# Optimization experiments

Hardware: AMD Instinct MI355X
Metric: run time of the kernel (lower is better)

The kernel has to match this reference:

```python
import jax, jax.numpy as jnp
import numpy as np

N_NODES = 25000
N_EDGES = 400000
EMBED_DIM = 128
NUM_HEADS = 8
D_K = EMBED_DIM // NUM_HEADS


def setup_inputs() -> dict:
    key = jax.random.key(0)
    ks = jax.random.split(key, 8)
    sc = 1.0 / np.sqrt(EMBED_DIM)
    return {
        "x": jax.random.normal(ks[0], (N_NODES, EMBED_DIM), jnp.float32),
        "edge_index": jax.random.randint(ks[1], (2, N_EDGES), 0, N_NODES),
        "attn_bias": jax.random.normal(ks[2], (N_EDGES, NUM_HEADS), jnp.float32),
        "Wq": jax.random.normal(ks[3], (EMBED_DIM, EMBED_DIM), jnp.float32) * sc,
        "bq": jnp.zeros((EMBED_DIM,), jnp.float32),
        "Wk": jax.random.normal(ks[4], (EMBED_DIM, EMBED_DIM), jnp.float32) * sc,
        "bk": jnp.zeros((EMBED_DIM,), jnp.float32),
        "Wv": jax.random.normal(ks[5], (EMBED_DIM, EMBED_DIM), jnp.float32) * sc,
        "bv": jnp.zeros((EMBED_DIM,), jnp.float32),
        "Wo": jax.random.normal(ks[6], (EMBED_DIM, EMBED_DIM), jnp.float32) * sc,
        "bo": jnp.zeros((EMBED_DIM,), jnp.float32),
    }


def reference(x, edge_index, attn_bias, Wq, bq, Wk, bk, Wv, bv, Wo, bo):
    N = x.shape[0]
    E = edge_index.shape[1]
    H, dk = NUM_HEADS, D_K
    scale = 1.0 / np.sqrt(dk).astype(np.float32)
    dst = edge_index[0]  # query/aggregation node per edge
    src = edge_index[1]  # key/value node per edge

    # project at node level (as torch: linear(x)[index]), then gather per edge
    q = (x @ Wq.T + bq)[dst].reshape(E, H, dk)
    k = (x @ Wk.T + bk)[src].reshape(E, H, dk)
    v = (x @ Wv.T + bv)[src].reshape(E, H, dk)

    logits = scale * jnp.sum(q * k, axis=2) + attn_bias  # [E, H]

    # segment softmax over edges grouped by destination node
    m = jax.ops.segment_max(logits, dst, num_segments=N)     # [N, H]
    e = jnp.exp(logits - m[dst])                              # [E, H]
    z = jax.ops.segment_sum(e, dst, num_segments=N)           # [N, H]
    scores = e / z[dst]                                       # [E, H]

    agg = jax.ops.segment_sum(scores[..., None] * v, dst, num_segments=N)  # [N, H, dk]
    out = agg.reshape(N, H * dk) @ Wo.T + bo                   # [N, embed_dim]
    return out, logits[..., None]
```

## Files before the change

kernel.cpp:

```cpp
#include <hip/hip_runtime.h>
#include <math.h>

#define N_NODES 25000
#define N_EDGES 400000
#define EMBED   128
#define HEADS   8
#define DK      16
#define NBLK    98

typedef __attribute__((ext_vector_type(8))) short bf16x8;
typedef __attribute__((ext_vector_type(4))) float f32x4;
typedef unsigned int uint;
typedef unsigned short ushort;

__device__ inline uint pack2_bf16(float a, float b) {
    union { float f; uint u; } ua, ub;
    ua.f = a; ub.f = b;
    uint ra = (ua.u + 0x7FFFu + ((ua.u >> 16) & 1u)) >> 16;
    uint rb = (ub.u + 0x7FFFu + ((ub.u >> 16) & 1u)) >> 16;
    return (ra & 0xFFFFu) | (rb << 16);
}
__device__ inline ushort cvt_bf16(float a) {
    union { float f; uint u; } ua; ua.f = a;
    return (ushort)((ua.u + 0x7FFFu + ((ua.u >> 16) & 1u)) >> 16);
}
__device__ inline float bf16_lo(uint u) {
    union { uint u; float f; } x; x.u = u << 16; return x.f;
}
__device__ inline float bf16_hi(uint u) {
    union { uint u; float f; } x; x.u = u & 0xFFFF0000u; return x.f;
}

#define NX (N_NODES * 128)
__global__ __launch_bounds__(256) void convert_all(
    const float* __restrict__ x,
    const float* __restrict__ Wq, const float* __restrict__ Wk,
    const float* __restrict__ Wv, const float* __restrict__ Wo,
    ushort* __restrict__ xb, ushort* __restrict__ wb, int* __restrict__ deg)
{
    int i = blockIdx.x * 256 + threadIdx.x;
    if (i < N_NODES) deg[i] = 0;
    int base = i * 2;
    if (base < NX) {
        float2 v = *reinterpret_cast<const float2*>(x + base);
        reinterpret_cast<uint*>(xb)[i] = pack2_bf16(v.x, v.y);
    } else {
        int j = base - NX;
        if (j < 4 * 16384) {
            const float* src = (j < 16384) ? Wq + j
                             : (j < 32768) ? Wk + (j - 16384)
                             : (j < 49152) ? Wv + (j - 32768)
                             :               Wo + (j - 49152);
            float2 v = *reinterpret_cast<const float2*>(src);
            reinterpret_cast<uint*>(wb)[j >> 1] = pack2_bf16(v.x, v.y);
        }
    }
}

__global__ __launch_bounds__(256) void gemm_qkv_deg(
    const ushort* __restrict__ A, const ushort* __restrict__ Wall,
    const float* __restrict__ bq, const float* __restrict__ bk,
    const float* __restrict__ bv,
    ushort* __restrict__ Qb, ushort* __restrict__ KVu,
    const int* __restrict__ ei, int* __restrict__ deg,
    int M)
{
    const int which = blockIdx.y;
    if (which == 3) {
        int t = blockIdx.x * 256 + threadIdx.x;
        int e = t * 4;
        if (e + 3 < N_EDGES) {
            int4 d = *reinterpret_cast<const int4*>(ei + e);
            atomicAdd(&deg[d.x], 1);
            atomicAdd(&deg[d.y], 1);
            atomicAdd(&deg[d.z], 1);
            atomicAdd(&deg[d.w], 1);
        } else {
            for (; e < N_EDGES && e < t * 4 + 4; ++e)
                atomicAdd(&deg[ei[e]], 1);
        }
        return;
    }

    const ushort* W = Wall + which * 16384;
    const float* bias = (which == 0) ? bq : (which == 1) ? bk : bv;

    const int lane = threadIdx.x & 63;
    const int wave = threadIdx.x >> 6;
    const int ml   = lane & 15;
    const int quad = lane >> 4;
    const int m0   = blockIdx.x * 64 + wave * 16;

    int arow = m0 + ml; if (arow >= M) arow = M - 1;
    const ushort* ap = A + arow * 128 + quad * 8;

    f32x4 acc[8];
#pragma unroll
    for (int ct = 0; ct < 8; ++ct) acc[ct] = (f32x4){0.f, 0.f, 0.f, 0.f};

#pragma unroll
    for (int ks = 0; ks < 128; ks += 32) {
        bf16x8 af = *reinterpret_cast<const bf16x8*>(ap + ks);
#pragma unroll
        for (int ct = 0; ct < 8; ++ct) {
            bf16x8 bf = *reinterpret_cast<const bf16x8*>(
                W + (ct * 16 + ml) * 128 + ks + quad * 8);
            acc[ct] = __builtin_amdgcn_mfma_f32_16x16x32_bf16(af, bf, acc[ct], 0, 0, 0);
        }
    }

#pragma unroll
    for (int ct = 0; ct < 8; ++ct) {
        int col = ct * 16 + ml;
        float bv_ = bias[col];
#pragma unroll
        for (int r = 0; r < 4; ++r) {
            int row = m0 + quad * 4 + r;
            if (row >= M) continue;
            ushort v = cvt_bf16(acc[ct][r] + bv_);
            if (which == 0) {
                Qb[row * 128 + col] = v;
            } else {
                KVu[row * 256 + (col >> 1) * 4 + (col & 1) + ((which == 2) ? 2 : 0)] = v;
            }
        }
    }
}

__global__ __launch_bounds__(256) void gemm_out(
    const ushort* __restrict__ A, const ushort* __restrict__ W,
    const float* __restrict__ bias, float* __restrict__ C, int M)
{
    const int lane = threadIdx.x & 63;
    const int wave = threadIdx.x >> 6;
    const int ml   = lane & 15;
    const int quad = lane >> 4;
    const int m0   = blockIdx.x * 64 + wave * 16;

    int arow = m0 + ml; if (arow >= M) arow = M - 1;
    const ushort* ap = A + arow * 128 + quad * 8;

    f32x4 acc[8];
#pragma unroll
    for (int ct = 0; ct < 8; ++ct) acc[ct] = (f32x4){0.f, 0.f, 0.f, 0.f};

#pragma unroll
    for (int ks = 0; ks < 128; ks += 32) {
        bf16x8 af = *reinterpret_cast<const bf16x8*>(ap + ks);
#pragma unroll
        for (int ct = 0; ct < 8; ++ct) {
            bf16x8 bf = *reinterpret_cast<const bf16x8*>(
                W + (ct * 16 + ml) * 128 + ks + quad * 8);
            acc[ct] = __builtin_amdgcn_mfma_f32_16x16x32_bf16(af, bf, acc[ct], 0, 0, 0);
        }
    }

#pragma unroll
    for (int ct = 0; ct < 8; ++ct) {
        int col = ct * 16 + ml;
        float bv_ = bias[col];
#pragma unroll
        for (int r = 0; r < 4; ++r) {
            int row = m0 + quad * 4 + r;
            if (row < M)
                C[row * 128 + col] = acc[ct][r] + bv_;
        }
    }
}

__global__ __launch_bounds__(256) void scan_blocks(
    const int* __restrict__ deg, int* __restrict__ excl, int* __restrict__ bsum)
{
    __shared__ int sh[256];
    int t = threadIdx.x;
    int gid = blockIdx.x * 256 + t;
    int v = (gid < N_NODES) ? deg[gid] : 0;
    sh[t] = v;
    __syncthreads();
#pragma unroll
    for (int off = 1; off < 256; off <<= 1) {
        int u = (t >= off) ? sh[t - off] : 0;
        __syncthreads();
        sh[t] += u;
        __syncthreads();
    }
    if (gid < N_NODES) excl[gid] = sh[t] - v;
    if (t == 255) bsum[blockIdx.x] = sh[255];
}

__global__ __launch_bounds__(128) void scan_tops(
    const int* __restrict__ bsum, int* __restrict__ bbase)
{
    __shared__ int sh[128];
    int t = threadIdx.x;
    int v = (t < NBLK) ? bsum[t] : 0;
    sh[t] = v;
    __syncthreads();
#pragma unroll
    for (int off = 1; off < 128; off <<= 1) {
        int u = (t >= off) ? sh[t - off] : 0;
        __syncthreads();
        sh[t] += u;
        __syncthreads();
    }
    if (t < NBLK) bbase[t] = sh[t] - v;
}

__global__ __launch_bounds__(256) void scan_apply(
    int* __restrict__ excl, const int* __restrict__ bbase,
    int* __restrict__ cursor)
{
    int t = threadIdx.x;
    int gid = blockIdx.x * 256 + t;
    if (gid < N_NODES) {
        int o = excl[gid] + bbase[blockIdx.x];
        excl[gid] = o;
        cursor[gid] = o;
    }
    if (blockIdx.x == 0 && t == 0) excl[N_NODES] = N_EDGES;
}

__global__ __launch_bounds__(256) void scatter_edges(
    const int* __restrict__ ei, int* __restrict__ cursor,
    int2* __restrict__ csr2)
{
    int e = blockIdx.x * 256 + threadIdx.x;
    if (e >= N_EDGES) return;
    int dst = ei[e];
    int src = ei[N_EDGES + e];
    int pos = atomicAdd(&cursor[dst], 1);
    csr2[pos] = make_int2(e, src);
}

__global__ __launch_bounds__(256) void fused_attn(
    const ushort* __restrict__ Q2, const uint2* __restrict__ KV,
    const float* __restrict__ attn_bias,
    const int* __restrict__ offsets, const int2* __restrict__ csr2,
    float* __restrict__ logits, ushort* __restrict__ AGG)
{
    const int lane = threadIdx.x & 63;
    const int wid  = threadIdx.x >> 6;
    const int n = blockIdx.x * 4 + wid;
    const int start = offsets[n], end = offsets[n + 1];
    const int h = lane >> 3;

    uint qu = reinterpret_cast<const uint*>(Q2)[n * 64 + lane];
    float qx = bf16_lo(qu), qy = bf16_hi(qu);

    float z = 0.f, accx = 0.f, accy = 0.f;

    for (int base = start; base < end; base += 64) {
        int cnt = end - base; if (cnt > 64) cnt = 64;
        int e_l = 0, s_l = 0;
        if (lane < cnt) {
            int2 es = csr2[base + lane];
            e_l = es.x; s_l = es.y;
        }
        int j = 0;
        for (; j + 3 < cnt; j += 4) {
            int e0 = __shfl(e_l, j, 64),     e1 = __shfl(e_l, j + 1, 64);
            int e2 = __shfl(e_l, j + 2, 64), e3 = __shfl(e_l, j + 3, 64);
            int s0 = __shfl(s_l, j, 64),     s1 = __shfl(s_l, j + 1, 64);
            int s2 = __shfl(s_l, j + 2, 64), s3 = __shfl(s_l, j + 3, 64);
            uint2 kv0 = KV[s0 * 64 + lane], kv1 = KV[s1 * 64 + lane];
            uint2 kv2 = KV[s2 * 64 + lane], kv3 = KV[s3 * 64 + lane];
            float b0 = attn_bias[e0 * 8 + h], b1 = attn_bias[e1 * 8 + h];
            float b2 = attn_bias[e2 * 8 + h], b3 = attn_bias[e3 * 8 + h];

            float d0 = qx * bf16_lo(kv0.x) + qy * bf16_hi(kv0.x);
            float d1 = qx * bf16_lo(kv1.x) + qy * bf16_hi(kv1.x);
            float d2 = qx * bf16_lo(kv2.x) + qy * bf16_hi(kv2.x);
            float d3 = qx * bf16_lo(kv3.x) + qy * bf16_hi(kv3.x);
#pragma unroll
            for (int off = 1; off < 8; off <<= 1) {
                d0 += __shfl_xor(d0, off, 64);
                d1 += __shfl_xor(d1, off, 64);
                d2 += __shfl_xor(d2, off, 64);
                d3 += __shfl_xor(d3, off, 64);
            }
            float l0 = 0.25f * d0 + b0, l1 = 0.25f * d1 + b1;
            float l2 = 0.25f * d2 + b2, l3 = 0.25f * d3 + b3;
            if ((lane & 7) == 0) {
                logits[e0 * 8 + h] = l0;
                logits[e1 * 8 + h] = l1;
                logits[e2 * 8 + h] = l2;
                logits[e3 * 8 + h] = l3;
            }
            float p0 = __expf(l0), p1 = __expf(l1);
            float p2 = __expf(l2), p3 = __expf(l3);
            z += (p0 + p1) + (p2 + p3);
            accx += p0 * bf16_lo(kv0.y) + p1 * bf16_lo(kv1.y)
                  + p2 * bf16_lo(kv2.y) + p3 * bf16_lo(kv3.y);
            accy += p0 * bf16_hi(kv0.y) + p1 * bf16_hi(kv1.y)
                  + p2 * bf16_hi(kv2.y) + p3 * bf16_hi(kv3.y);
        }
        for (; j < cnt; ++j) {
            int e0 = __shfl(e_l, j, 64);
            int s0 = __shfl(s_l, j, 64);
            uint2 kv0 = KV[s0 * 64 + lane];
            float b0 = attn_bias[e0 * 8 + h];
            float d0 = qx * bf16_lo(kv0.x) + qy * bf16_hi(kv0.x);
#pragma unroll
            for (int off = 1; off < 8; off <<= 1) d0 += __shfl_xor(d0, off, 64);
            float l0 = 0.25f * d0 + b0;
            if ((lane & 7) == 0) logits[e0 * 8 + h] = l0;
            float p0 = __expf(l0);
            z += p0;
            accx += p0 * bf16_lo(kv0.y);
            accy += p0 * bf16_hi(kv0.y);
        }
    }

    float inv = (z > 0.f) ? 1.f / z : 0.f;
    reinterpret_cast<uint*>(AGG)[n * 64 + lane] = pack2_bf16(accx * inv, accy * inv);
}

extern "C" void kernel_launch(void* const* d_in, const int* in_sizes, int n_in,
                              void* d_out, int out_size, void* d_ws, size_t ws_size,
                              hipStream_t stream)
{
    const float* x         = (const float*)d_in[0];
    const int*   ei        = (const int*)  d_in[1];
    const float* attn_bias = (const float*)d_in[2];
    const float* Wq = (const float*)d_in[3];
    const float* bq = (const float*)d_in[4];
    const float* Wk = (const float*)d_in[5];
    const float* bk = (const float*)d_in[6];
    const float* Wv = (const float*)d_in[7];
    const float* bv = (const float*)d_in[8];
    const float* Wo = (const float*)d_in[9];
    const float* bo = (const float*)d_in[10];

    float* out    = (float*)d_out;
    float* logits = out + N_NODES * EMBED;

    ushort* xb   = (ushort*)d_ws;
    ushort* wb   = xb + NX;
    ushort* Qb   = wb + 4 * 16384;
    ushort* KVu  = Qb + NX;
    ushort* AGGb = KVu + 2 * NX;
    int* deg     = (int*)(AGGb + NX);
    int* offsets = deg + N_NODES;
    int* cursor  = offsets + N_NODES + 1;
    int2* csr2   = (int2*)(cursor + N_NODES);
    int* bsum    = (int*)(csr2 + N_EDGES);
    int* bbase   = bsum + NBLK;

    int npairs = (NX + 4 * 16384) / 2;
    convert_all<<<(npairs + 255) / 256, 256, 0, stream>>>(x, Wq, Wk, Wv, Wo, xb, wb, deg);

    int gblocks = (N_NODES + 63) / 64;
    dim3 qkvgrid(gblocks, 4);
    gemm_qkv_deg<<<qkvgrid, 256, 0, stream>>>(xb, wb, bq, bk, bv, Qb, KVu,
                                              ei, deg, N_NODES);

    scan_blocks<<<NBLK, 256, 0, stream>>>(deg, offsets, bsum);
    scan_tops<<<1, 128, 0, stream>>>(bsum, bbase);
    scan_apply<<<NBLK, 256, 0, stream>>>(offsets, bbase, cursor);
    scatter_edges<<<(N_EDGES + 255) / 256, 256, 0, stream>>>(ei, cursor, csr2);

    fused_attn<<<N_NODES / 4, 256, 0, stream>>>(Qb, (const uint2*)KVu, attn_bias,
                                                offsets, csr2, logits, AGGb);

    gemm_out<<<gblocks, 256, 0, stream>>>(AGGb, wb + 3 * 16384, bo, out, N_NODES);
}
```

Measured before the change: 214.0 us.

## Process eight edges per wave with per-head lanes and separate K/V buffers

Splits the interleaved KV buffer into separate K and V arrays and remaps fused_attn so each lane owns one head of one of eight concurrent edges. Each lane now loads a full 16-element K and V slice with 128-bit loads and computes the dot product locally, with no shuffle reduction per edge. Partial sums are combined once at the end with a transpose-style butterfly reduction. This removes per-edge shuffles and serial edge iteration, at the cost of more registers per lane and wasted lanes for nodes whose degree is not a multiple of eight.

```diff
diff --git a/kernel.cpp b/kernel.cpp
--- a/kernel.cpp
+++ b/kernel.cpp
@@ -61,7 +61,7 @@
     const ushort* __restrict__ A, const ushort* __restrict__ Wall,
     const float* __restrict__ bq, const float* __restrict__ bk,
     const float* __restrict__ bv,
-    ushort* __restrict__ Qb, ushort* __restrict__ KVu,
+    ushort* __restrict__ Qb, ushort* __restrict__ Kb, ushort* __restrict__ Vb,
     const int* __restrict__ ei, int* __restrict__ deg,
     int M)
 {
@@ -84,6 +84,7 @@
 
     const ushort* W = Wall + which * 16384;
     const float* bias = (which == 0) ? bq : (which == 1) ? bk : bv;
+    ushort* C = (which == 0) ? Qb : (which == 1) ? Kb : Vb;
 
     const int lane = threadIdx.x & 63;
     const int wave = threadIdx.x >> 6;
@@ -116,13 +117,8 @@
 #pragma unroll
         for (int r = 0; r < 4; ++r) {
             int row = m0 + quad * 4 + r;
-            if (row >= M) continue;
-            ushort v = cvt_bf16(acc[ct][r] + bv_);
-            if (which == 0) {
-                Qb[row * 128 + col] = v;
-            } else {
-                KVu[row * 256 + (col >> 1) * 4 + (col & 1) + ((which == 2) ? 2 : 0)] = v;
-            }
+            if (row < M)
+                C[row * 128 + col] = cvt_bf16(acc[ct][r] + bv_);
         }
     }
 }
@@ -233,7 +229,8 @@
 }
 
 __global__ __launch_bounds__(256) void fused_attn(
-    const ushort* __restrict__ Q2, const uint2* __restrict__ KV,
+    const ushort* __restrict__ Q2, const ushort* __restrict__ K2,
+    const ushort* __restrict__ V2,
     const float* __restrict__ attn_bias,
     const int* __restrict__ offsets, const int2* __restrict__ csr2,
     float* __restrict__ logits, ushort* __restrict__ AGG)
@@ -242,77 +239,95 @@
     const int wid  = threadIdx.x >> 6;
     const int n = blockIdx.x * 4 + wid;
     const int start = offsets[n], end = offsets[n + 1];
-    const int h = lane >> 3;
-
-    uint qu = reinterpret_cast<const uint*>(Q2)[n * 64 + lane];
-    float qx = bf16_lo(qu), qy = bf16_hi(qu);
-
-    float z = 0.f, accx = 0.f, accy = 0.f;
-
-    for (int base = start; base < end; base += 64) {
-        int cnt = end - base; if (cnt > 64) cnt = 64;
-        int e_l = 0, s_l = 0;
-        if (lane < cnt) {
-            int2 es = csr2[base + lane];
-            e_l = es.x; s_l = es.y;
-        }
-        int j = 0;
-        for (; j + 3 < cnt; j += 4) {
-            int e0 = __shfl(e_l, j, 64),     e1 = __shfl(e_l, j + 1, 64);
-            int e2 = __shfl(e_l, j + 2, 64), e3 = __shfl(e_l, j + 3, 64);
-            int s0 = __shfl(s_l, j, 64),     s1 = __shfl(s_l, j + 1, 64);
-            int s2 = __shfl(s_l, j + 2, 64), s3 = __shfl(s_l, j + 3, 64);
-            uint2 kv0 = KV[s0 * 64 + lane], kv1 = KV[s1 * 64 + lane];
-            uint2 kv2 = KV[s2 * 64 + lane], kv3 = KV[s3 * 64 + lane];
-            float b0 = attn_bias[e0 * 8 + h], b1 = attn_bias[e1 * 8 + h];
-            float b2 = attn_bias[e2 * 8 + h], b3 = attn_bias[e3 * 8 + h];
-
-            float d0 = qx * bf16_lo(kv0.x) + qy * bf16_hi(kv0.x);
-            float d1 = qx * bf16_lo(kv1.x) + qy * bf16_hi(kv1.x);
-            float d2 = qx * bf16_lo(kv2.x) + qy * bf16_hi(kv2.x);
-            float d3 = qx * bf16_lo(kv3.x) + qy * bf16_hi(kv3.x);
-#pragma unroll
-            for (int off = 1; off < 8; off <<= 1) {
-                d0 += __shfl_xor(d0, off, 64);
-                d1 += __shfl_xor(d1, off, 64);
-                d2 += __shfl_xor(d2, off, 64);
-                d3 += __shfl_xor(d3, off, 64);
-            }
-            float l0 = 0.25f * d0 + b0, l1 = 0.25f * d1 + b1;
-            float l2 = 0.25f * d2 + b2, l3 = 0.25f * d3 + b3;
-            if ((lane & 7) == 0) {
-                logits[e0 * 8 + h] = l0;
-                logits[e1 * 8 + h] = l1;
-                logits[e2 * 8 + h] = l2;
-                logits[e3 * 8 + h] = l3;
-            }
-            float p0 = __expf(l0), p1 = __expf(l1);
-            float p2 = __expf(l2), p3 = __expf(l3);
-            z += (p0 + p1) + (p2 + p3);
-            accx += p0 * bf16_lo(kv0.y) + p1 * bf16_lo(kv1.y)
-                  + p2 * bf16_lo(kv2.y) + p3 * bf16_lo(kv3.y);
-            accy += p0 * bf16_hi(kv0.y) + p1 * bf16_hi(kv1.y)
-                  + p2 * bf16_hi(kv2.y) + p3 * bf16_hi(kv3.y);
-        }
-        for (; j < cnt; ++j) {
-            int e0 = __shfl(e_l, j, 64);
-            int s0 = __shfl(s_l, j, 64);
-            uint2 kv0 = KV[s0 * 64 + lane];
-            float b0 = attn_bias[e0 * 8 + h];
-            float d0 = qx * bf16_lo(kv0.x) + qy * bf16_hi(kv0.x);
-#pragma unroll
-            for (int off = 1; off < 8; off <<= 1) d0 += __shfl_xor(d0, off, 64);
-            float l0 = 0.25f * d0 + b0;
-            if ((lane & 7) == 0) logits[e0 * 8 + h] = l0;
-            float p0 = __expf(l0);
-            z += p0;
-            accx += p0 * bf16_lo(kv0.y);
-            accy += p0 * bf16_hi(kv0.y);
-        }
-    }
+    const int h  = lane & 7;
+    const int es = lane >> 3;
+
+    const uint4* Qu4 = reinterpret_cast<const uint4*>(Q2);
+    const uint4* Ku4 = reinterpret_cast<const uint4*>(K2);
+    const uint4* Vu4 = reinterpret_cast<const uint4*>(V2);
+
+    uint4 qa = Qu4[n * 16 + h * 2];
+    uint4 qb = Qu4[n * 16 + h * 2 + 1];
+    float qf[16];
+    {
+        uint qq[8] = {qa.x, qa.y, qa.z, qa.w, qb.x, qb.y, qb.z, qb.w};
+#pragma unroll
+        for (int j = 0; j < 8; ++j) {
+            qf[2 * j]     = bf16_lo(qq[j]);
+            qf[2 * j + 1] = bf16_hi(qq[j]);
+        }
+    }
+
+    float acc[16];
+#pragma unroll
+    for (int j = 0; j < 16; ++j) acc[j] = 0.f;
+    float z = 0.f;
+
+    for (int base = start; base < end; base += 8) {
+        bool valid = (base + es) < end;
+        int idx = base + es; if (!valid) idx = end - 1;
+        int2 epair = csr2[idx];
+        int e = epair.x, s = epair.y;
+
+        uint4 k0 = Ku4[s * 16 + h * 2];
+        uint4 k1 = Ku4[s * 16 + h * 2 + 1];
+        uint4 v0 = Vu4[s * 16 + h * 2];
+        uint4 v1 = Vu4[s * 16 + h * 2 + 1];
+        float bias = attn_bias[e * 8 + h];
+
+        uint kk[8] = {k0.x, k0.y, k0.z, k0.w, k1.x, k1.y, k1.z, k1.w};
+        float d = 0.f;
+#pragma unroll
+        for (int j = 0; j < 8; ++j)
+            d += qf[2 * j] * bf16_lo(kk[j]) + qf[2 * j + 1] * bf16_hi(kk[j]);
+
+        float l = 0.25f * d + bias;
+        float p = 0.f;
+        if (valid) {
+            logits[e * 8 + h] = l;
+            p = __expf(l);
+        }
+        z += p;
+
+        uint vv[8] = {v0.x, v0.y, v0.z, v0.w, v1.x, v1.y, v1.z, v1.w};
+#pragma unroll
+        for (int j = 0; j < 8; ++j) {
+            acc[2 * j]     += p * bf16_lo(vv[j]);
+            acc[2 * j + 1] += p * bf16_hi(vv[j]);
+        }
+    }
+
+    {
+        int bit = (lane >> 5) & 1;
+#pragma unroll
+        for (int j = 0; j < 8; ++j) {
+            float send = bit ? acc[j] : acc[j + 8];
+            float keep = bit ? acc[j + 8] : acc[j];
+            acc[j] = keep + __shfl_xor(send, 32, 64);
+        }
+        bit = (lane >> 4) & 1;
+#pragma unroll
+        for (int j = 0; j < 4; ++j) {
+            float send = bit ? acc[j] : acc[j + 4];
+            float keep = bit ? acc[j + 4] : acc[j];
+            acc[j] = keep + __shfl_xor(send, 16, 64);
+        }
+        bit = (lane >> 3) & 1;
+#pragma unroll
+        for (int j = 0; j < 2; ++j) {
+            float send = bit ? acc[j] : acc[j + 2];
+            float keep = bit ? acc[j + 2] : acc[j];
+            acc[j] = keep + __shfl_xor(send, 8, 64);
+        }
+    }
+    z += __shfl_xor(z, 8, 64);
+    z += __shfl_xor(z, 16, 64);
+    z += __shfl_xor(z, 32, 64);
 
     float inv = (z > 0.f) ? 1.f / z : 0.f;
-    reinterpret_cast<uint*>(AGG)[n * 64 + lane] = pack2_bf16(accx * inv, accy * inv);
+    int d_off = ((lane >> 5) & 1) * 8 + ((lane >> 4) & 1) * 4 + ((lane >> 3) & 1) * 2;
+    reinterpret_cast<uint*>(AGG)[n * 64 + h * 8 + (d_off >> 1)] =
+        pack2_bf16(acc[0] * inv, acc[1] * inv);
 }
 
 extern "C" void kernel_launch(void* const* d_in, const int* in_sizes, int n_in,
@@ -337,8 +352,9 @@
     ushort* xb   = (ushort*)d_ws;
     ushort* wb   = xb + NX;
     ushort* Qb   = wb + 4 * 16384;
-    ushort* KVu  = Qb + NX;
-    ushort* AGGb = KVu + 2 * NX;
+    ushort* Kb   = Qb + NX;
+    ushort* Vb   = Kb + NX;
+    ushort* AGGb = Vb + NX;
     int* deg     = (int*)(AGGb + NX);
     int* offsets = deg + N_NODES;
     int* cursor  = offsets + N_NODES + 1;
@@ -351,7 +367,7 @@
 
     int gblocks = (N_NODES + 63) / 64;
     dim3 qkvgrid(gblocks, 4);
-    gemm_qkv_deg<<<qkvgrid, 256, 0, stream>>>(xb, wb, bq, bk, bv, Qb, KVu,
+    gemm_qkv_deg<<<qkvgrid, 256, 0, stream>>>(xb, wb, bq, bk, bv, Qb, Kb, Vb,
                                               ei, deg, N_NODES);
 
     scan_blocks<<<NBLK, 256, 0, stream>>>(deg, offsets, bsum);
@@ -359,7 +375,7 @@
     scan_apply<<<NBLK, 256, 0, stream>>>(offsets, bbase, cursor);
     scatter_edges<<<(N_EDGES + 255) / 256, 256, 0, stream>>>(ei, cursor, csr2);
 
-    fused_attn<<<N_NODES / 4, 256, 0, stream>>>(Qb, (const uint2*)KVu, attn_bias,
+    fused_attn<<<N_NODES / 4, 256, 0, stream>>>(Qb, Kb, Vb, attn_bias,
                                                 offsets, csr2, logits, AGGb);
 
     gemm_out<<<gblocks, 256, 0, stream>>>(AGGb, wb + 3 * 16384, bo, out, N_NODES);
```

After: 210.1 us. No clear change (-1.8%).
